# Performance work log

Measured on AMD Instinct MI355X. Metric: run time of the kernel, lower is better.

Reference implementation:

```python
import jax, jax.numpy as jnp
import numpy as np

D_CONV = 4
D_STATE = 16
DT_RANK = 64  # ceil(1024/16)


def _forward(x, W_in, conv_w, conv_b, W_x, W_dt, b_dt, A_log, Dp, W_out):
    B, L, Dm = x.shape
    d_inner = W_dt.shape[0]
    # in_proj: (B,L,Dm) @ (2*d_inner, Dm)^T
    xz = jnp.einsum('bld,ed->ble', x, W_in)
    xc, z = jnp.split(xz, 2, axis=-1)  # each (B,L,d_inner)
    # depthwise causal conv1d (torch pads both sides by d_conv-1 then truncates to L == left-pad only)
    xt = jnp.swapaxes(xc, 1, 2)  # (B, d_inner, L)
    conv = jax.lax.conv_general_dilated(
        xt, conv_w[:, None, :], window_strides=(1,),
        padding=[(D_CONV - 1, 0)], feature_group_count=d_inner)
    xconv = jax.nn.silu(jnp.swapaxes(conv, 1, 2) + conv_b)  # (B,L,d_inner)
    # x_proj -> dt_low, B, C
    x_dbl = jnp.einsum('bld,ed->ble', xconv, W_x)
    dt_low = x_dbl[..., :DT_RANK]
    Bp = x_dbl[..., DT_RANK:DT_RANK + D_STATE]      # (B,L,N)
    Cp = x_dbl[..., DT_RANK + D_STATE:]             # (B,L,N)
    dt = jax.nn.softplus(jnp.einsum('blr,dr->bld', dt_low, W_dt) + b_dt)  # (B,L,d_inner)
    A = -jnp.exp(A_log)  # (d_inner, N)

    # recurrence h_t = exp(dt_t * A) * h_{t-1} + dt_t * B_t * x_t ; y_t = <h_t, C_t>
    def step(h, inp):
        dt_t, B_t, C_t, x_t = inp  # (B,D),(B,N),(B,N),(B,D)
        dA = jnp.exp(dt_t[..., None] * A)                      # (B,D,N)
        dBx = dt_t[..., None] * B_t[:, None, :] * x_t[..., None]
        h = dA * h + dBx
        y = jnp.einsum('bdn,bn->bd', h, C_t)
        return h, y

    h0 = jnp.zeros((B, d_inner, D_STATE), dtype=x.dtype)
    xs = (jnp.swapaxes(dt, 0, 1), jnp.swapaxes(Bp, 0, 1),
          jnp.swapaxes(Cp, 0, 1), jnp.swapaxes(xconv, 0, 1))
    _, ys = jax.lax.scan(step, h0, xs)  # ys: (L,B,d_inner)
    y = jnp.swapaxes(ys, 0, 1) + xconv * Dp  # skip connection with D
    out = jnp.einsum('bld,ed->ble', y * jax.nn.silu(z), W_out)
    return out


def setup_inputs() -> dict:
    key = jax.random.key(0)
    ks = jax.random.split(key, 8)
    B, L, d_model = 2, 1024, 1024
    d_inner = 2 * d_model
    x = jax.random.normal(ks[0], (B, L, d_model), dtype=jnp.float32)
    W_in = jax.random.normal(ks[1], (2 * d_inner, d_model), dtype=jnp.float32) / np.sqrt(d_model)
    conv_w = jax.random.normal(ks[2], (d_inner, D_CONV), dtype=jnp.float32) / np.sqrt(D_CONV)
    conv_b = jnp.zeros((d_inner,), dtype=jnp.float32)
    W_x = jax.random.normal(ks[3], (DT_RANK + 2 * D_STATE, d_inner), dtype=jnp.float32) / np.sqrt(d_inner)
    W_dt = jax.random.uniform(ks[4], (d_inner, DT_RANK), minval=-1.0, maxval=1.0, dtype=jnp.float32) * DT_RANK ** -0.5
    dt = jnp.exp(jax.random.uniform(ks[5], (d_inner,), dtype=jnp.float32)
                 * (np.log(0.1) - np.log(0.001)) + np.log(0.001))
    b_dt = dt + jnp.log(-jnp.expm1(-dt))  # softplus inverse init
    A_log = jnp.log(jnp.tile(jnp.arange(1, D_STATE + 1, dtype=jnp.float32), (d_inner, 1)))
    Dp = jnp.ones((d_inner,), dtype=jnp.float32)
    W_out = jax.random.normal(ks[6], (d_model, d_inner), dtype=jnp.float32) / np.sqrt(d_inner)
    return {'x': x, 'W_in': W_in, 'conv_w': conv_w, 'conv_b': conv_b, 'W_x': W_x,
            'W_dt': W_dt, 'b_dt': b_dt, 'A_log': A_log, 'Dp': Dp, 'W_out': W_out}


def reference(x, W_in, conv_w, conv_b, W_x, W_dt, b_dt, A_log, Dp, W_out):
    return _forward(x, W_in, conv_w, conv_b, W_x, W_dt, b_dt, A_log, Dp, W_out)
```

## Files before the change

### kernel.cpp

```cpp
#include <hip/hip_runtime.h>
#include <hip/hip_bf16.h>
#include <math.h>

constexpr int Bb  = 2;
constexpr int Ls  = 1024;
constexpr int DM  = 1024;
constexpr int DI  = 2048;
constexpr int DXZ = 4096;
constexpr int DXD = 96;
constexpr int DTR = 64;
constexpr int DST = 16;
constexpr int NCH = 16;
constexpr int CHL = 64;
constexpr int ML  = Bb * Ls;

typedef __attribute__((ext_vector_type(8))) short bf16x8;
typedef __attribute__((ext_vector_type(4))) float f32x4;

__device__ __forceinline__ float sigmoidf_(float v) {
    return 1.0f / (1.0f + __expf(-v));
}

__device__ __forceinline__ int pk_bf16(float lo, float hi) {
    unsigned int ul = __float_as_uint(lo);
    ul += 0x7fffu + ((ul >> 16) & 1u);
    unsigned int uh = __float_as_uint(hi);
    uh += 0x7fffu + ((uh >> 16) & 1u);
    return (int)((ul >> 16) | (uh & 0xffff0000u));
}

template <int CTRL>
__device__ __forceinline__ float dpp_add_(float v) {
    int t = __builtin_amdgcn_update_dpp(
        0, __float_as_int(v), CTRL, 0xF, 0xF, true);
    return v + __int_as_float(t);
}
__device__ __forceinline__ float red16_(float p) {
    p = dpp_add_<0xB1>(p);
    p = dpp_add_<0x4E>(p);
    p = dpp_add_<0x141>(p);
    p = dpp_add_<0x140>(p);
    return p;
}

__device__ __forceinline__ int swz(int row, int chunk) {
    return (((row << 2) + chunk) ^ (row & 7)) << 3;
}

__global__ __launch_bounds__(256) void cvt_bf16_kernel(
    const float* __restrict__ in, unsigned short* __restrict__ out, int n4)
{
    const int i = blockIdx.x * 256 + threadIdx.x;
    if (i >= n4) return;
    const float4 v = *(const float4*)(in + (size_t)i * 4);
    *(int2*)(out + (size_t)i * 4) =
        make_int2(pk_bf16(v.x, v.y), pk_bf16(v.z, v.w));
}

template <int SPLIT, int ABF16, int WBF16>
__global__ __launch_bounds__(256) void gemm_bf16_f32in(
    const void* __restrict__ Av, int lda,
    const void* __restrict__ Wv, int ldw,
    float* __restrict__ C, float* __restrict__ C2, int ldc, int K,
    int za, int zw, long zc)
{
    __shared__ __align__(16) unsigned short As[128 * 32];
    __shared__ __align__(16) unsigned short Ws[128 * 32];

    const int tid  = threadIdx.x;
    const int lane = tid & 63;
    const int wave = tid >> 6;
    const int bm = blockIdx.y * 128;
    const int bn = blockIdx.x * 128;
    const int z  = blockIdx.z;
    C += (size_t)z * zc;

    const int srow = tid >> 1;
    const int cb   = (tid & 1) * 2;
    const float* Ag = (ABF16 ? nullptr
        : (const float*)Av + (size_t)z * za + (size_t)(bm + srow) * lda + cb * 8);
    const unsigned short* Ag16 = (ABF16
        ? (const unsigned short*)Av + (size_t)z * za
          + (size_t)(bm + srow) * lda + cb * 8 : nullptr);
    const float* Wg = (WBF16 ? nullptr
        : (const float*)Wv + (size_t)z * zw + (size_t)(bn + srow) * ldw + cb * 8);
    const unsigned short* Wg16 = (WBF16
        ? (const unsigned short*)Wv + (size_t)z * zw
          + (size_t)(bn + srow) * ldw + cb * 8 : nullptr);
    const int ia0 = swz(srow, cb);
    const int ia1 = swz(srow, cb + 1);

    const int wr = (wave >> 1) * 64;
    const int wc = (wave & 1) * 64;
    const int fr = lane & 15;
    const int fq = lane >> 4;

    f32x4 acc[4][4];
#pragma unroll
    for (int m = 0; m < 4; ++m)
#pragma unroll
        for (int n = 0; n < 4; ++n) acc[m][n] = (f32x4){0.f, 0.f, 0.f, 0.f};

    for (int k0 = 0; k0 < K; k0 += 32) {
        int4 pa0, pa1, pw0, pw1;
        if (ABF16) {
            pa0 = *(const int4*)(Ag16 + k0);
            pa1 = *(const int4*)(Ag16 + k0 + 8);
        } else {
            const float4 a0 = *(const float4*)(Ag + k0);
            const float4 a1 = *(const float4*)(Ag + k0 + 4);
            const float4 a2 = *(const float4*)(Ag + k0 + 8);
            const float4 a3 = *(const float4*)(Ag + k0 + 12);
            pa0 = (int4){pk_bf16(a0.x, a0.y), pk_bf16(a0.z, a0.w),
                         pk_bf16(a1.x, a1.y), pk_bf16(a1.z, a1.w)};
            pa1 = (int4){pk_bf16(a2.x, a2.y), pk_bf16(a2.z, a2.w),
                         pk_bf16(a3.x, a3.y), pk_bf16(a3.z, a3.w)};
        }
        if (WBF16) {
            pw0 = *(const int4*)(Wg16 + k0);
            pw1 = *(const int4*)(Wg16 + k0 + 8);
        } else {
            const float4 w0 = *(const float4*)(Wg + k0);
            const float4 w1 = *(const float4*)(Wg + k0 + 4);
            const float4 w2 = *(const float4*)(Wg + k0 + 8);
            const float4 w3 = *(const float4*)(Wg + k0 + 12);
            pw0 = (int4){pk_bf16(w0.x, w0.y), pk_bf16(w0.z, w0.w),
                         pk_bf16(w1.x, w1.y), pk_bf16(w1.z, w1.w)};
            pw1 = (int4){pk_bf16(w2.x, w2.y), pk_bf16(w2.z, w2.w),
                         pk_bf16(w3.x, w3.y), pk_bf16(w3.z, w3.w)};
        }

        __syncthreads();
        *(int4*)(As + ia0) = pa0;
        *(int4*)(As + ia1) = pa1;
        *(int4*)(Ws + ia0) = pw0;
        *(int4*)(Ws + ia1) = pw1;
        __syncthreads();

        bf16x8 af[4], bfv[4];
#pragma unroll
        for (int m = 0; m < 4; ++m)
            af[m] = *(const bf16x8*)(As + swz(wr + m * 16 + fr, fq));
#pragma unroll
        for (int n = 0; n < 4; ++n)
            bfv[n] = *(const bf16x8*)(Ws + swz(wc + n * 16 + fr, fq));
#pragma unroll
        for (int m = 0; m < 4; ++m)
#pragma unroll
            for (int n = 0; n < 4; ++n)
                acc[m][n] = __builtin_amdgcn_mfma_f32_16x16x32_bf16(
                    af[m], bfv[n], acc[m][n], 0, 0, 0);
    }

#pragma unroll
    for (int m = 0; m < 4; ++m)
#pragma unroll
        for (int n = 0; n < 4; ++n) {
            const int col = bn + wc + n * 16 + fr;
#pragma unroll
            for (int j = 0; j < 4; ++j) {
                const int row = bm + wr + m * 16 + fq * 4 + j;
                const float v = acc[m][n][j];
                if (SPLIT) {
                    if (col < DI) {
                        C[(size_t)row * ldc + col] = v;
                    } else {
                        C2[(size_t)row * ldc + (col - DI)] = v * sigmoidf_(v);
                    }
                } else {
                    C[(size_t)row * ldc + col] = v;
                }
            }
        }
}

__global__ __launch_bounds__(256) void reduce4_kernel(
    const float* __restrict__ part, float* __restrict__ out, int n4)
{
    const int i = blockIdx.x * 256 + threadIdx.x;
    if (i >= n4) return;
    const size_t stride = (size_t)ML * DM;
    float4 a = *(const float4*)(part + (size_t)i * 4);
    const float4 b = *(const float4*)(part + stride + (size_t)i * 4);
    const float4 c = *(const float4*)(part + 2 * stride + (size_t)i * 4);
    const float4 d = *(const float4*)(part + 3 * stride + (size_t)i * 4);
    a.x += b.x + c.x + d.x;
    a.y += b.y + c.y + d.y;
    a.z += b.z + c.z + d.z;
    a.w += b.w + c.w + d.w;
    *(float4*)(out + (size_t)i * 4) = a;
}

template <int EPI, int ATRANS>
__global__ __launch_bounds__(256) void gemm_nt(
    const float* __restrict__ A, int lda,
    const float* __restrict__ W, int ldw,
    float* __restrict__ C, int ldc,
    int N, int K, const float* __restrict__ bias, int za, int zw, int zc)
{
    A += (size_t)blockIdx.z * za;
    W += (size_t)blockIdx.z * zw;
    C += (size_t)blockIdx.z * zc;

    __shared__ float Asl[16][132];
    __shared__ float Wsl[16][132];

    const int tid = threadIdx.x;
    const int tx = tid & 15;
    const int ty = tid >> 4;
    const int bm = blockIdx.y * 128;
    const int bn = blockIdx.x * 128;

    const int lr = tid >> 1;
    const int lk = (tid & 1) * 8;
    const int krow = tid >> 4;
    const int mseg = (tid & 15) * 8;

    float acc[8][8];
#pragma unroll
    for (int i = 0; i < 8; ++i)
#pragma unroll
        for (int j = 0; j < 8; ++j) acc[i][j] = 0.0f;

    const float* Ap = ATRANS
        ? A + (size_t)krow * lda + bm + mseg
        : A + (size_t)(bm + lr) * lda + lk;
    const float* Wp = W + (size_t)(bn + lr) * ldw + lk;
    const bool wok = (bn + lr) < N;
    const float4 f4z = make_float4(0.f, 0.f, 0.f, 0.f);

    for (int k0 = 0; k0 < K; k0 += 16) {
        float4 av0, av1;
        if (ATRANS) {
            av0 = *(const float4*)(Ap + (size_t)k0 * lda);
            av1 = *(const float4*)(Ap + (size_t)k0 * lda + 4);
        } else {
            av0 = *(const float4*)(Ap + k0);
            av1 = *(const float4*)(Ap + k0 + 4);
        }
        const float4 wv0 = wok ? *(const float4*)(Wp + k0)     : f4z;
        const float4 wv1 = wok ? *(const float4*)(Wp + k0 + 4) : f4z;

        __syncthreads();
        if (ATRANS) {
            *(float4*)&Asl[krow][mseg]     = av0;
            *(float4*)&Asl[krow][mseg + 4] = av1;
        } else {
            Asl[lk + 0][lr] = av0.x; Asl[lk + 1][lr] = av0.y;
            Asl[lk + 2][lr] = av0.z; Asl[lk + 3][lr] = av0.w;
            Asl[lk + 4][lr] = av1.x; Asl[lk + 5][lr] = av1.y;
            Asl[lk + 6][lr] = av1.z; Asl[lk + 7][lr] = av1.w;
        }
        Wsl[lk + 0][lr] = wv0.x; Wsl[lk + 1][lr] = wv0.y;
        Wsl[lk + 2][lr] = wv0.z; Wsl[lk + 3][lr] = wv0.w;
        Wsl[lk + 4][lr] = wv1.x; Wsl[lk + 5][lr] = wv1.y;
        Wsl[lk + 6][lr] = wv1.z; Wsl[lk + 7][lr] = wv1.w;
        __syncthreads();

#pragma unroll
        for (int k = 0; k < 16; ++k) {
            const float4 a0 = *(const float4*)&Asl[k][(ty << 2)];
            const float4 a1 = *(const float4*)&Asl[k][64 + (ty << 2)];
            const float4 b0 = *(const float4*)&Wsl[k][(tx << 2)];
            const float4 b1 = *(const float4*)&Wsl[k][64 + (tx << 2)];
            const float ar[8] = {a0.x, a0.y, a0.z, a0.w, a1.x, a1.y, a1.z, a1.w};
            const float br[8] = {b0.x, b0.y, b0.z, b0.w, b1.x, b1.y, b1.z, b1.w};
#pragma unroll
            for (int i = 0; i < 8; ++i)
#pragma unroll
                for (int j = 0; j < 8; ++j)
                    acc[i][j] = fmaf(ar[i], br[j], acc[i][j]);
        }
    }

#pragma unroll
    for (int i = 0; i < 8; ++i) {
        const int row = bm + ((i & 4) << 4) + (ty << 2) + (i & 3);
#pragma unroll
        for (int j = 0; j < 8; ++j) {
            const int col = bn + ((j & 4) << 4) + (tx << 2) + (j & 3);
            if (col < N) {
                float v = acc[i][j];
                if (EPI == 2) {
                    v += bias[row];
                    v = (v > 20.f) ? v : log1pf(__expf(v));
                }
                C[(size_t)row * ldc + col] = v;
            }
        }
    }
}

__global__ __launch_bounds__(256) void reduce_xdbl_kernel(
    const float* __restrict__ part, float* __restrict__ dtlow,
    float* __restrict__ bcT)
{
    const int idx = blockIdx.x * 256 + threadIdx.x;
    if (idx >= ML * DXD) return;
    const int m = idx / DXD;
    const int j = idx - m * DXD;
    const float* p = part + (size_t)m * 768 + j;
    float s = 0.0f;
#pragma unroll
    for (int kc = 0; kc < 8; ++kc) s += p[kc * DXD];
    if (j < DTR) dtlow[(size_t)m * DTR + j] = s;
    else         bcT[(size_t)(j - DTR) * ML + m] = s;
}

constexpr int CT_LDS = 260;
__global__ __launch_bounds__(256) void conv_transpose_kernel(
    const float* __restrict__ xc,
    const float* __restrict__ conv_w,
    const float* __restrict__ conv_b,
    float* __restrict__ xT)
{
    __shared__ float tile[32][CT_LDS];
    const int d0 = blockIdx.x * 32;
    const int m0 = blockIdx.y * 256;
    const int t  = threadIdx.x;
    const bool atStart = ((m0 & (Ls - 1)) == 0);

    for (int rg = 0; rg < 33; ++rg) {
        const int r = rg * 8 + (t >> 5) - 3;
        const int dcol = t & 31;
        if (r <= 255) {
            float v = 0.0f;
            if (r >= 0 || !atStart)
                v = xc[(size_t)(m0 + r) * DI + d0 + dcol];
            tile[dcol][3 + r] = v;
        }
    }
    __syncthreads();

    const int dd  = t >> 3;
    const int seg = (t & 7) * 32;
    const int d   = d0 + dd;
    const float4 cw = *(const float4*)(conv_w + (d << 2));
    const float  cb = conv_b[d];
    float* dst = xT + (size_t)d * ML + m0 + seg;

    float4 cur = *(const float4*)&tile[dd][seg];
#pragma unroll
    for (int g = 0; g < 8; ++g) {
        const float4 nxt = *(const float4*)&tile[dd][seg + 4 * g + 4];
        const float a0 = cb + cw.x*cur.x + cw.y*cur.y + cw.z*cur.z + cw.w*cur.w;
        const float a1 = cb + cw.x*cur.y + cw.y*cur.z + cw.z*cur.w + cw.w*nxt.x;
        const float a2 = cb + cw.x*cur.z + cw.y*cur.w + cw.z*nxt.x + cw.w*nxt.y;
        const float a3 = cb + cw.x*cur.w + cw.y*nxt.x + cw.z*nxt.y + cw.w*nxt.z;
        float4 o;
        o.x = a0 * sigmoidf_(a0); o.y = a1 * sigmoidf_(a1);
        o.z = a2 * sigmoidf_(a2); o.w = a3 * sigmoidf_(a3);
        *(float4*)(dst + 4 * g) = o;
        cur = nxt;
    }
}

__global__ __launch_bounds__(256) void scan_pass1(
    const float* __restrict__ dtT,
    const float* __restrict__ xT,
    const float* __restrict__ bcT,
    const float* __restrict__ A_log,
    float* __restrict__ hend, float* __restrict__ Dprod)
{
    const int b    = blockIdx.z;
    const int c    = blockIdx.y;
    const int lane = threadIdx.x & 63;
    const int wave = threadIdx.x >> 6;
    const int n    = lane & 15;
    const int dl   = lane >> 4;
    const int d    = blockIdx.x * 16 + wave * 4 + dl;
    const int m0   = b * Ls + c * CHL;

    const float Anat = -__expf(A_log[(d << 4) + n]);

    const float4* dtp = (const float4*)(dtT + (size_t)d * ML + m0);
    const float4* xp  = (const float4*)(xT  + (size_t)d * ML + m0);
    const float4* Bp  = (const float4*)(bcT + (size_t)n * ML + m0);

    float4 dt4 = dtp[0], x4 = xp[0], B4 = Bp[0];
    float h = 0.0f, S = 0.0f;

    for (int it = 0; it < CHL / 4; ++it) {
        const float4 dtc = dt4, xc4 = x4, Bc = B4;
        if (it + 1 < CHL / 4) {
            dt4 = dtp[it + 1]; x4 = xp[it + 1]; B4 = Bp[it + 1];
        }
#pragma unroll
        for (int i = 0; i < 4; ++i) {
            const float dtv = ((const float*)&dtc)[i];
            const float xv  = ((const float*)&xc4)[i];
            const float Bn  = ((const float*)&Bc)[i];
            S += dtv;
            const float e = __expf(dtv * Anat);
            h = fmaf(e, h, dtv * xv * Bn);
        }
    }

    const size_t idx = (((size_t)(b * NCH + c) * DI + d) << 4) + n;
    hend[idx]  = h;
    Dprod[idx] = __expf(Anat * S);
}

__global__ __launch_bounds__(256) void scan_pass2(
    const float* __restrict__ dtT,
    float* xT,
    const float* __restrict__ bcT,
    const float* __restrict__ A_log,
    const float* __restrict__ Dp,
    const float* __restrict__ hend, const float* __restrict__ Dprod)
{
    const int b    = blockIdx.z;
    const int c    = blockIdx.y;
    const int lane = threadIdx.x & 63;
    const int wave = threadIdx.x >> 6;
    const int n    = lane & 15;
    const int dl   = lane >> 4;
    const int d    = blockIdx.x * 16 + wave * 4 + dl;
    const int m0   = b * Ls + c * CHL;

    const float Anat = -__expf(A_log[(d << 4) + n]);
    const float dpd  = Dp[d];

    float h = 0.0f;
    for (int cp = 0; cp < c; ++cp) {
        const size_t off = (((size_t)(b * NCH + cp) * DI + d) << 4) + n;
        h = fmaf(Dprod[off], h, hend[off]);
    }

    const float4* dtp = (const float4*)(dtT + (size_t)d * ML + m0);
    const float4* xp  = (const float4*)(xT  + (size_t)d * ML + m0);
    const float4* Bp  = (const float4*)(bcT + (size_t)n * ML + m0);
    const float4* Cp  = (const float4*)(bcT + (size_t)(DST + n) * ML + m0);
    float4* yq = (float4*)(xT + (size_t)d * ML + m0);

    float4 dt4 = dtp[0], x4 = xp[0], B4 = Bp[0], C4 = Cp[0];

    for (int it = 0; it < CHL / 4; ++it) {
        const float4 dtc = dt4, xc4 = x4, Bc = B4, Cc = C4;
        if (it + 1 < CHL / 4) {
            dt4 = dtp[it + 1]; x4 = xp[it + 1];
            B4 = Bp[it + 1];   C4 = Cp[it + 1];
        }
        float4 y4;
#pragma unroll
        for (int i = 0; i < 4; ++i) {
            const float dtv = ((const float*)&dtc)[i];
            const float xv  = ((const float*)&xc4)[i];
            const float Bn  = ((const float*)&Bc)[i];
            const float Cn  = ((const float*)&Cc)[i];
            const float e = __expf(dtv * Anat);
            h = fmaf(e, h, dtv * xv * Bn);
            const float p = red16_(h * Cn);
            ((float*)&y4)[i] = fmaf(xv, dpd, p);
        }
        if (n == 0) yq[it] = y4;
    }
}

__global__ __launch_bounds__(256) void gate_transpose_kernel(
    const float* __restrict__ yT,
    const float* __restrict__ zg,
    unsigned short* __restrict__ yb)
{
    __shared__ float Ty[64][65];
    __shared__ float Tz[64][65];
    const int d0 = blockIdx.x * 64;
    const int m0 = blockIdx.y * 64;
    const int t  = threadIdx.x;
    const int cc = t & 63, r4 = t >> 6;

#pragma unroll 4
    for (int rr = 0; rr < 16; ++rr) {
        const int r = rr * 4 + r4;
        Ty[r][cc] = yT[(size_t)(d0 + r) * ML + m0 + cc];
        Tz[r][cc] = zg[(size_t)(m0 + r) * DI + d0 + cc];
    }
    __syncthreads();

    const int dp  = (t & 31) * 2;
    const int mr4 = t >> 5;
#pragma unroll 4
    for (int rr = 0; rr < 8; ++rr) {
        const int mr = rr * 8 + mr4;
        const float v0 = Ty[dp][mr]     * Tz[mr][dp];
        const float v1 = Ty[dp + 1][mr] * Tz[mr][dp + 1];
        *(unsigned int*)(yb + (size_t)(m0 + mr) * DI + d0 + dp) =
            (unsigned int)pk_bf16(v0, v1);
    }
}

extern "C" void kernel_launch(void* const* d_in, const int* in_sizes, int n_in,
                              void* d_out, int out_size, void* d_ws, size_t ws_size,
                              hipStream_t stream)
{
    const float* x      = (const float*)d_in[0];
    const float* W_in   = (const float*)d_in[1];
    const float* conv_w = (const float*)d_in[2];
    const float* conv_b = (const float*)d_in[3];
    const float* W_x    = (const float*)d_in[4];
    const float* W_dt   = (const float*)d_in[5];
    const float* b_dt   = (const float*)d_in[6];
    const float* A_log  = (const float*)d_in[7];
    const float* Dp     = (const float*)d_in[8];
    const float* W_out  = (const float*)d_in[9];
    float* out = (float*)d_out;

    float* ws     = (float*)d_ws;
    float* xc_arr = ws;
    float* zg_arr = xc_arr + (size_t)ML * DI;
    float* xT_arr = zg_arr + (size_t)ML * DI;
    float* dtlow  = xT_arr + (size_t)ML * DI;
    float* bcT    = dtlow  + (size_t)ML * DTR;

    float* hend  = out;
    float* Dprod = hend + (size_t)Bb * NCH * DI * DST;

    unsigned short* xbf  = (unsigned short*)xT_arr;
    unsigned short* wibf = xbf + (size_t)ML * DM;
    float* dtT = xc_arr;
    unsigned short* ybf  = (unsigned short*)xc_arr;
    unsigned short* wobf = (unsigned short*)xc_arr + (size_t)ML * DI;
    float* oPart = zg_arr;

    const dim3 blk(256);

    cvt_bf16_kernel<<<dim3(ML * DM / 4 / 256), blk, 0, stream>>>(
        x, xbf, ML * DM / 4);
    cvt_bf16_kernel<<<dim3(DXZ * DM / 4 / 256), blk, 0, stream>>>(
        W_in, wibf, DXZ * DM / 4);

    gemm_bf16_f32in<1, 1, 1><<<dim3(DXZ / 128, ML / 128), blk, 0, stream>>>(
        xbf, DM, wibf, DM, xc_arr, zg_arr, DI, DM, 0, 0, 0);

    conv_transpose_kernel<<<dim3(DI / 32, ML / 256), blk, 0, stream>>>(
        xc_arr, conv_w, conv_b, xT_arr);

    gemm_nt<0, 1><<<dim3(1, ML / 128, 8), blk, 0, stream>>>(
        xT_arr, ML, W_x, DI, xc_arr, 768, DXD, DI / 8, nullptr,
        (DI / 8) * ML, DI / 8, DXD);
    reduce_xdbl_kernel<<<dim3((ML * DXD + 255) / 256), blk, 0, stream>>>(
        xc_arr, dtlow, bcT);

    gemm_nt<2, 0><<<dim3(ML / 128, DI / 128), blk, 0, stream>>>(
        W_dt, DTR, dtlow, DTR, dtT, ML, ML, DTR, b_dt, 0, 0, 0);

    scan_pass1<<<dim3(DI / 16, NCH - 1, Bb), blk, 0, stream>>>(
        dtT, xT_arr, bcT, A_log, hend, Dprod);
    scan_pass2<<<dim3(DI / 16, NCH, Bb), blk, 0, stream>>>(
        dtT, xT_arr, bcT, A_log, Dp, hend, Dprod);

    gate_transpose_kernel<<<dim3(DI / 64, ML / 64), blk, 0, stream>>>(
        xT_arr, zg_arr, ybf);
    cvt_bf16_kernel<<<dim3(DM * DI / 4 / 256), blk, 0, stream>>>(
        W_out, wobf, DM * DI / 4);

    gemm_bf16_f32in<0, 1, 1><<<dim3(DM / 128, ML / 128, 4), blk, 0, stream>>>(
        ybf, DI, wobf, DI, oPart, nullptr, DM, DI / 4,
        DI / 4, DI / 4, (long)ML * DM);

    reduce4_kernel<<<dim3((ML * DM / 4 + 255) / 256), blk, 0, stream>>>(
        oPart, out, ML * DM / 4);
}
```

Before: 409.2 us.

## Narrow GEMM N-tile to 64, halve scan chunk count, deepen scan prefetch

The bf16 GEMM template is simplified to bf16-only inputs and gains a configurable N-tile width. Both the in_proj and out_proj launches now use 64-wide tiles, which doubles the block count for better occupancy but lowers data reuse per block. The chunked scan switches from 16 chunks of 64 to 8 chunks of 128, which cuts the serial cross-chunk prefix work and the number of pass-1 launches at the cost of less parallelism. The scan loops also prefetch two float4 groups ahead instead of one, to hide more load latency.

```diff
diff --git a/kernel.cpp b/kernel.cpp
--- a/kernel.cpp
+++ b/kernel.cpp
@@ -10,8 +10,8 @@
 constexpr int DXD = 96;
 constexpr int DTR = 64;
 constexpr int DST = 16;
-constexpr int NCH = 16;
-constexpr int CHL = 64;
+constexpr int NCH = 8;
+constexpr int CHL = 128;
 constexpr int ML  = Bb * Ls;
 
 typedef __attribute__((ext_vector_type(8))) short bf16x8;
@@ -57,97 +57,75 @@
         make_int2(pk_bf16(v.x, v.y), pk_bf16(v.z, v.w));
 }
 
-template <int SPLIT, int ABF16, int WBF16>
-__global__ __launch_bounds__(256) void gemm_bf16_f32in(
-    const void* __restrict__ Av, int lda,
-    const void* __restrict__ Wv, int ldw,
+template <int SPLIT, int BNT>
+__global__ __launch_bounds__(256) void gemm_bf16bf16(
+    const unsigned short* __restrict__ A, int lda,
+    const unsigned short* __restrict__ W, int ldw,
     float* __restrict__ C, float* __restrict__ C2, int ldc, int K,
     int za, int zw, long zc)
 {
+    constexpr int NACC = BNT / 32;
     __shared__ __align__(16) unsigned short As[128 * 32];
-    __shared__ __align__(16) unsigned short Ws[128 * 32];
+    __shared__ __align__(16) unsigned short Ws[BNT * 32];
 
     const int tid  = threadIdx.x;
     const int lane = tid & 63;
     const int wave = tid >> 6;
     const int bm = blockIdx.y * 128;
-    const int bn = blockIdx.x * 128;
+    const int bn = blockIdx.x * BNT;
     const int z  = blockIdx.z;
     C += (size_t)z * zc;
 
     const int srow = tid >> 1;
     const int cb   = (tid & 1) * 2;
-    const float* Ag = (ABF16 ? nullptr
-        : (const float*)Av + (size_t)z * za + (size_t)(bm + srow) * lda + cb * 8);
-    const unsigned short* Ag16 = (ABF16
-        ? (const unsigned short*)Av + (size_t)z * za
-          + (size_t)(bm + srow) * lda + cb * 8 : nullptr);
-    const float* Wg = (WBF16 ? nullptr
-        : (const float*)Wv + (size_t)z * zw + (size_t)(bn + srow) * ldw + cb * 8);
-    const unsigned short* Wg16 = (WBF16
-        ? (const unsigned short*)Wv + (size_t)z * zw
-          + (size_t)(bn + srow) * ldw + cb * 8 : nullptr);
+    const unsigned short* Ag = A + (size_t)z * za
+        + (size_t)(bm + srow) * lda + cb * 8;
     const int ia0 = swz(srow, cb);
     const int ia1 = swz(srow, cb + 1);
 
+    const int srW = (BNT == 128) ? (tid >> 1) : (tid >> 2);
+    const int cbW = (BNT == 128) ? (tid & 1) * 2 : (tid & 3);
+    const unsigned short* Wg = W + (size_t)z * zw
+        + (size_t)(bn + srW) * ldw + cbW * 8;
+    const int iw0 = swz(srW, cbW);
+    const int iw1 = (BNT == 128) ? swz(srW, cbW + 1) : 0;
+
     const int wr = (wave >> 1) * 64;
-    const int wc = (wave & 1) * 64;
+    const int wc = (wave & 1) * (BNT / 2);
     const int fr = lane & 15;
     const int fq = lane >> 4;
 
-    f32x4 acc[4][4];
+    f32x4 acc[4][NACC];
 #pragma unroll
     for (int m = 0; m < 4; ++m)
 #pragma unroll
-        for (int n = 0; n < 4; ++n) acc[m][n] = (f32x4){0.f, 0.f, 0.f, 0.f};
+        for (int n = 0; n < NACC; ++n) acc[m][n] = (f32x4){0.f, 0.f, 0.f, 0.f};
 
     for (int k0 = 0; k0 < K; k0 += 32) {
-        int4 pa0, pa1, pw0, pw1;
-        if (ABF16) {
-            pa0 = *(const int4*)(Ag16 + k0);
-            pa1 = *(const int4*)(Ag16 + k0 + 8);
-        } else {
-            const float4 a0 = *(const float4*)(Ag + k0);
-            const float4 a1 = *(const float4*)(Ag + k0 + 4);
-            const float4 a2 = *(const float4*)(Ag + k0 + 8);
-            const float4 a3 = *(const float4*)(Ag + k0 + 12);
-            pa0 = (int4){pk_bf16(a0.x, a0.y), pk_bf16(a0.z, a0.w),
-                         pk_bf16(a1.x, a1.y), pk_bf16(a1.z, a1.w)};
-            pa1 = (int4){pk_bf16(a2.x, a2.y), pk_bf16(a2.z, a2.w),
-                         pk_bf16(a3.x, a3.y), pk_bf16(a3.z, a3.w)};
-        }
-        if (WBF16) {
-            pw0 = *(const int4*)(Wg16 + k0);
-            pw1 = *(const int4*)(Wg16 + k0 + 8);
-        } else {
-            const float4 w0 = *(const float4*)(Wg + k0);
-            const float4 w1 = *(const float4*)(Wg + k0 + 4);
-            const float4 w2 = *(const float4*)(Wg + k0 + 8);
-            const float4 w3 = *(const float4*)(Wg + k0 + 12);
-            pw0 = (int4){pk_bf16(w0.x, w0.y), pk_bf16(w0.z, w0.w),
-                         pk_bf16(w1.x, w1.y), pk_bf16(w1.z, w1.w)};
-            pw1 = (int4){pk_bf16(w2.x, w2.y), pk_bf16(w2.z, w2.w),
-                         pk_bf16(w3.x, w3.y), pk_bf16(w3.z, w3.w)};
-        }
+        const int4 pa0 = *(const int4*)(Ag + k0);
+        const int4 pa1 = *(const int4*)(Ag + k0 + 8);
+        const int4 pw0 = *(const int4*)(Wg + k0);
+        int4 pw1;
+        if (BNT == 128) pw1 = *(const int4*)(Wg + k0 + 8);
 
         __syncthreads();
         *(int4*)(As + ia0) = pa0;
         *(int4*)(As + ia1) = pa1;
-        *(int4*)(Ws + ia0) = pw0;
-        *(int4*)(Ws + ia1) = pw1;
+        *(int4*)(Ws + iw0) = pw0;
+        if (BNT == 128) *(int4*)(Ws + iw1) = pw1;
         __syncthreads();
 
-        bf16x8 af[4], bfv[4];
+        bf16x8 af[4], bfv[NACC];
 #pragma unroll
         for (int m = 0; m < 4; ++m)
             af[m] = *(const bf16x8*)(As + swz(wr + m * 16 + fr, fq));
 #pragma unroll
-        for (int n = 0; n < 4; ++n)
+        for (int n = 0; n < NACC; ++n)
             bfv[n] = *(const bf16x8*)(Ws + swz(wc + n * 16 + fr, fq));
 #pragma unroll
         for (int m = 0; m < 4; ++m)
 #pragma unroll
-            for (int n = 0; n < 4; ++n)
+            for (int n = 0; n < NACC; ++n)
                 acc[m][n] = __builtin_amdgcn_mfma_f32_16x16x32_bf16(
                     af[m], bfv[n], acc[m][n], 0, 0, 0);
     }
@@ -155,7 +133,7 @@
 #pragma unroll
     for (int m = 0; m < 4; ++m)
 #pragma unroll
-        for (int n = 0; n < 4; ++n) {
+        for (int n = 0; n < NACC; ++n) {
             const int col = bn + wc + n * 16 + fr;
 #pragma unroll
             for (int j = 0; j < 4; ++j) {
@@ -377,13 +355,15 @@
     const float4* xp  = (const float4*)(xT  + (size_t)d * ML + m0);
     const float4* Bp  = (const float4*)(bcT + (size_t)n * ML + m0);
 
-    float4 dt4 = dtp[0], x4 = xp[0], B4 = Bp[0];
+    float4 dtA = dtp[0], xA = xp[0], BA = Bp[0];
+    float4 dtB = dtp[1], xB = xp[1], BB = Bp[1];
     float h = 0.0f, S = 0.0f;
 
     for (int it = 0; it < CHL / 4; ++it) {
-        const float4 dtc = dt4, xc4 = x4, Bc = B4;
-        if (it + 1 < CHL / 4) {
-            dt4 = dtp[it + 1]; x4 = xp[it + 1]; B4 = Bp[it + 1];
+        const float4 dtc = dtA, xc4 = xA, Bc = BA;
+        dtA = dtB; xA = xB; BA = BB;
+        if (it + 2 < CHL / 4) {
+            dtB = dtp[it + 2]; xB = xp[it + 2]; BB = Bp[it + 2];
         }
 #pragma unroll
         for (int i = 0; i < 4; ++i) {
@@ -433,13 +413,15 @@
     const float4* Cp  = (const float4*)(bcT + (size_t)(DST + n) * ML + m0);
     float4* yq = (float4*)(xT + (size_t)d * ML + m0);
 
-    float4 dt4 = dtp[0], x4 = xp[0], B4 = Bp[0], C4 = Cp[0];
+    float4 dtA = dtp[0], xA = xp[0], BA = Bp[0], CA = Cp[0];
+    float4 dtB = dtp[1], xB = xp[1], BB = Bp[1], CB = Cp[1];
 
     for (int it = 0; it < CHL / 4; ++it) {
-        const float4 dtc = dt4, xc4 = x4, Bc = B4, Cc = C4;
-        if (it + 1 < CHL / 4) {
-            dt4 = dtp[it + 1]; x4 = xp[it + 1];
-            B4 = Bp[it + 1];   C4 = Cp[it + 1];
+        const float4 dtc = dtA, xc4 = xA, Bc = BA, Cc = CA;
+        dtA = dtB; xA = xB; BA = BB; CA = CB;
+        if (it + 2 < CHL / 4) {
+            dtB = dtp[it + 2]; xB = xp[it + 2];
+            BB = Bp[it + 2];   CB = Cp[it + 2];
         }
         float4 y4;
 #pragma unroll
@@ -529,7 +511,7 @@
     cvt_bf16_kernel<<<dim3(DXZ * DM / 4 / 256), blk, 0, stream>>>(
         W_in, wibf, DXZ * DM / 4);
 
-    gemm_bf16_f32in<1, 1, 1><<<dim3(DXZ / 128, ML / 128), blk, 0, stream>>>(
+    gemm_bf16bf16<1, 64><<<dim3(DXZ / 64, ML / 128), blk, 0, stream>>>(
         xbf, DM, wibf, DM, xc_arr, zg_arr, DI, DM, 0, 0, 0);
 
     conv_transpose_kernel<<<dim3(DI / 32, ML / 256), blk, 0, stream>>>(
@@ -554,7 +536,7 @@
     cvt_bf16_kernel<<<dim3(DM * DI / 4 / 256), blk, 0, stream>>>(
         W_out, wobf, DM * DI / 4);
 
-    gemm_bf16_f32in<0, 1, 1><<<dim3(DM / 128, ML / 128, 4), blk, 0, stream>>>(
+    gemm_bf16bf16<0, 64><<<dim3(DM / 64, ML / 128, 4), blk, 0, stream>>>(
         ybf, DI, wobf, DI, oPart, nullptr, DM, DI / 4,
         DI / 4, DI / 4, (long)ML * DM);
 
```

New measurement: 478.4 us. +16.9%, slower.
